# Kernel optimization log

Measured on AMD Instinct MI355X. Metric: run time of the kernel, lower is better.

Reference implementation:

```python
import jax, jax.numpy as jnp
import numpy as np

NEG = -9.0e9  # the -9000000000.0 sentinel used by the torch code


def _masked_bidir_scores(first, second, fmask, smask):
    """Vectorized form of the BxB python double loop in score_grounding.
    first: (B,N,D), second: (B,L,D), fmask: (B,N), smask: (B,L).
    Returns sent_scores (B,B) and mention_scores (B,N,L) (= diagonal att)."""
    mask = fmask[:, None, :, None] * smask[None, :, None, :]          # (B,B,N,L)
    avg = jnp.where(mask != 0, mask, NEG)
    am_first = jax.nn.softmax(avg, axis=2)                            # softmax over N (dim=0 per pair)
    am_second = jax.nn.softmax(avg, axis=3)                           # softmax over L (dim=1 per pair)
    dot = jnp.einsum('ind,jld->ijnl', first, second)                  # (B,B,N,L)
    attm = dot * mask
    att = jnp.where(attm * mask != 0, attm, NEG)
    aw_first = jax.nn.softmax(att, axis=3) * mask                     # softmax(att, dim=-1)*mask
    aw_second = jnp.transpose(
        jax.nn.softmax(jnp.swapaxes(att, 2, 3), axis=3) * jnp.swapaxes(mask, 2, 3), (0, 1, 3, 2)
    )                                                                 # softmax(att.T,-1)*mask.T, transposed back
    sent = (jnp.sum(aw_first * att * am_first, axis=(2, 3))
            + jnp.sum(aw_second * att * am_second, axis=(2, 3)))      # (B,B)
    B = first.shape[0]
    mention = att[jnp.arange(B), jnp.arange(B)]                       # diagonal pairs (B,N,L)
    return sent, mention


def _pairwise_mlp(first, second, W1, b1, W2, b2, W3, b3):
    # SimplePairWiseClassifier: MLP over cat(first, second, first*second); dropout=0 (eval-deterministic)
    x = jnp.concatenate([first, second, first * second], axis=-1)     # (..., 3D)
    h = jax.nn.relu(x @ W1 + b1)
    h = jax.nn.relu(h @ W2 + b2)
    return (h @ W3 + b3)[..., 0]


def setup_inputs() -> dict:
    key = jax.random.key(0)
    ks = jax.random.split(key, 12)
    B, Nt, Ns, L, D, H = 32, 64, 48, 36, 1024, 1024

    def mask(k, n):
        m = (jax.random.uniform(k, (B, n)) < 0.85).astype(jnp.float32)
        return m.at[:, :2].set(1.0)  # guarantee no all-zero rows

    return {
        'text_embeddings': jax.random.normal(ks[0], (B, Nt, D), jnp.float32),
        'span_embeddings': jax.random.normal(ks[1], (B, Ns, D), jnp.float32),
        'image_embeddings': jax.random.normal(ks[2], (B, L, D), jnp.float32),
        'text_mask': mask(ks[3], Nt),
        'span_mask': mask(ks[4], Ns),
        'image_mask': mask(ks[5], L),
        'W1': jax.random.normal(ks[6], (3 * D, H), jnp.float32) * 0.02,
        'b1': jnp.zeros((H,), jnp.float32),
        'W2': jax.random.normal(ks[7], (H, H), jnp.float32) * 0.02,
        'b2': jnp.zeros((H,), jnp.float32),
        'W3': jax.random.normal(ks[8], (H, 1), jnp.float32) * 0.02,
        'b3': jnp.zeros((1,), jnp.float32),
    }


def reference(text_embeddings, span_embeddings, image_embeddings,
              text_mask, span_mask, image_mask, W1, b1, W2, b2, W3, b3):
    B, Ns, D = span_embeddings.shape
    # calculate_loss
    S, _ = _masked_bidir_scores(text_embeddings, image_embeddings, text_mask, image_mask)
    # span_emb.view(B, N, -1, D).mean(dim=2) is identity for (B,Ns,D)
    _, grounding_scores = _masked_bidir_scores(span_embeddings, image_embeddings, span_mask, image_mask)
    # score_text over all span pairs (itertools.combinations order == triu_indices k=1)
    fi, si = np.triu_indices(Ns, k=1)
    text_scores = _pairwise_mlp(span_embeddings[:, fi], span_embeddings[:, si],
                                W1, b1, W2, b2, W3, b3)               # (B, Ns*(Ns-1)/2)
    # contrastive retrieval loss over the BxB sentence-image score matrix
    loss = -(jnp.trace(jax.nn.log_softmax(S, axis=1))
             + jnp.trace(jax.nn.log_softmax(S.T, axis=1))) / B
    return loss, grounding_scores, text_scores
```

## Files before the change

### kernel.cpp

```cpp
#include <hip/hip_runtime.h>
#include <math.h>
#include <stdint.h>

#define B_    32
#define NT    64
#define NS    48
#define LI    36
#define D_    1024
#define H_    1024
#define NPAIR 1128
#define ROWS  (B_*NPAIR)
#define NEGV  -9.0e9f
#define NROWT 282
#define CPX   36

typedef _Float16 half8 __attribute__((ext_vector_type(8)));
typedef float floatx4 __attribute__((ext_vector_type(4)));
typedef __attribute__((address_space(3))) uint32_t lds_u32;
typedef __attribute__((address_space(1))) const uint32_t glb_u32;

#define GLOAD16(src, dst) __builtin_amdgcn_global_load_lds((glb_u32*)(src), (lds_u32*)(dst), 16, 0, 0)

template<int EPI, int REMAP>
__global__ __launch_bounds__(256) void mfma_gemm(
    const _Float16* __restrict__ A, const _Float16* __restrict__ Bt,
    float* __restrict__ Cf, float* __restrict__ scores,
    const float* __restrict__ bias, const float* __restrict__ W3,
    int N, int K) {
  __shared__ __align__(16) _Float16 sA[8192];
  __shared__ __align__(16) _Float16 sB[8192];
  __shared__ float sRed[128][2];
  int rowT, colT;
  if (REMAP) {
    int bid = blockIdx.x;
    int x = bid & 7, ord = bid >> 3;
    rowT = x * CPX + (ord >> 3);
    colT = ord & 7;
    if (rowT >= NROWT) return;
  } else {
    rowT = blockIdx.y; colT = blockIdx.x;
  }
  const int rowBase = rowT * 128, colBase = colT * 128;
  const int tid = threadIdx.x;
  const int lane = tid & 63;
  const int wave = tid >> 6;
  const int wr = wave >> 1, wc = wave & 1;
  const int l15 = lane & 15, l16 = lane >> 4;

  const int sRow = tid >> 2;
  const int sCol = (tid & 3) << 3;
  const _Float16* gA = A + (size_t)(rowBase + sRow) * K + sCol;
  const _Float16* gB = Bt + (size_t)(colBase + sRow) * K + sCol;
  _Float16* lA = sA + tid * 8;
  _Float16* lB = sB + tid * 8;

  floatx4 acc[4][4] = {};
  for (int k0 = 0; k0 < K; k0 += 64) {
    GLOAD16(gA + k0,              lA);
    GLOAD16(gA + 64 * K + k0,     lA + 2048);
    GLOAD16(gA + k0 + 32,         lA + 4096);
    GLOAD16(gA + 64 * K + k0 + 32,lA + 6144);
    GLOAD16(gB + k0,              lB);
    GLOAD16(gB + 64 * K + k0,     lB + 2048);
    GLOAD16(gB + k0 + 32,         lB + 4096);
    GLOAD16(gB + 64 * K + k0 + 32,lB + 6144);
    __syncthreads();
#pragma unroll
    for (int h = 0; h < 2; ++h) {
      const int hb = h * 4096;
      half8 aF[4], bF[4];
#pragma unroll
      for (int i = 0; i < 4; ++i)
        aF[i] = *(const half8*)&sA[hb + (wr * 64 + i * 16 + l15) * 32 + l16 * 8];
#pragma unroll
      for (int j = 0; j < 4; ++j)
        bF[j] = *(const half8*)&sB[hb + (wc * 64 + j * 16 + l15) * 32 + l16 * 8];
#pragma unroll
      for (int i = 0; i < 4; ++i)
#pragma unroll
        for (int j = 0; j < 4; ++j)
          acc[i][j] = __builtin_amdgcn_mfma_f32_16x16x32_f16(aF[i], bF[j], acc[i][j], 0, 0, 0);
    }
    __syncthreads();
  }

  if (EPI == 0) {
#pragma unroll
    for (int i = 0; i < 4; ++i)
#pragma unroll
      for (int q = 0; q < 4; ++q) {
        int r = rowBase + wr * 64 + i * 16 + l16 * 4 + q;
#pragma unroll
        for (int j = 0; j < 4; ++j) {
          int c = colBase + wc * 64 + j * 16 + l15;
          Cf[(size_t)r * N + c] = acc[i][j][q];
        }
      }
  } else {
    float bv[4], wv[4];
#pragma unroll
    for (int j = 0; j < 4; ++j) {
      int c = colBase + wc * 64 + j * 16 + l15;
      bv[j] = bias[c];
      wv[j] = W3[c];
    }
#pragma unroll
    for (int i = 0; i < 4; ++i)
#pragma unroll
      for (int q = 0; q < 4; ++q) {
        float s = 0.f;
#pragma unroll
        for (int j = 0; j < 4; ++j) s += fmaxf(acc[i][j][q] + bv[j], 0.f) * wv[j];
        s += __shfl_xor(s, 1); s += __shfl_xor(s, 2);
        s += __shfl_xor(s, 4); s += __shfl_xor(s, 8);
        if (l15 == 0) sRed[wr * 64 + i * 16 + l16 * 4 + q][wc] = s;
      }
    __syncthreads();
    if (tid < 128)
      atomicAdd(&scores[rowBase + tid], sRed[tid][0] + sRed[tid][1]);
  }
}

__global__ __launch_bounds__(256) void gemm1_fused(
    const _Float16* __restrict__ spanH, const _Float16* __restrict__ W1cT,
    const float* __restrict__ AB1, const float* __restrict__ b1,
    _Float16* __restrict__ h1out,
    const int* __restrict__ idxF, const int* __restrict__ idxS) {
  __shared__ __align__(16) _Float16 sA[8192];
  __shared__ __align__(16) _Float16 sB[8192];
  __shared__ int sIF[128], sIS[128];
  int bid = blockIdx.x;
  int x = bid & 7, ord = bid >> 3;
  int rowT = x * CPX + (ord >> 3);
  int colT = ord & 7;
  if (rowT >= NROWT) return;
  const int rowBase = rowT * 128, colBase = colT * 128;
  const int tid = threadIdx.x;
  const int lane = tid & 63;
  const int wave = tid >> 6;
  const int wr = wave >> 1, wc = wave & 1;
  const int l15 = lane & 15, l16 = lane >> 4;

  if (tid < 128) {
    int rg = rowBase + tid;
    sIF[tid] = idxF[rg];
    sIS[tid] = idxS[rg];
  }
  __syncthreads();

  const int sRow = tid >> 2;
  const int sCol = (tid & 3) << 3;
  const _Float16* gB = W1cT + (size_t)(colBase + sRow) * D_ + sCol;
  _Float16* lB = sB + tid * 8;
  const _Float16* pf0 = spanH + (size_t)sIF[sRow] * D_ + sCol;
  const _Float16* ps0 = spanH + (size_t)sIS[sRow] * D_ + sCol;
  const _Float16* pf1 = spanH + (size_t)sIF[sRow + 64] * D_ + sCol;
  const _Float16* ps1 = spanH + (size_t)sIS[sRow + 64] * D_ + sCol;

  floatx4 acc[4][4] = {};
  for (int k0 = 0; k0 < D_; k0 += 64) {
    GLOAD16(gB + k0,               lB);
    GLOAD16(gB + 64 * D_ + k0,     lB + 2048);
    GLOAD16(gB + k0 + 32,          lB + 4096);
    GLOAD16(gB + 64 * D_ + k0 + 32,lB + 6144);
    half8 f00 = *(const half8*)(pf0 + k0);
    half8 s00 = *(const half8*)(ps0 + k0);
    half8 f10 = *(const half8*)(pf1 + k0);
    half8 s10 = *(const half8*)(ps1 + k0);
    half8 f01 = *(const half8*)(pf0 + k0 + 32);
    half8 s01 = *(const half8*)(ps0 + k0 + 32);
    half8 f11 = *(const half8*)(pf1 + k0 + 32);
    half8 s11 = *(const half8*)(ps1 + k0 + 32);
    *(half8*)(sA + tid * 8)        = f00 * s00;
    *(half8*)(sA + 2048 + tid * 8) = f10 * s10;
    *(half8*)(sA + 4096 + tid * 8) = f01 * s01;
    *(half8*)(sA + 6144 + tid * 8) = f11 * s11;
    __syncthreads();
#pragma unroll
    for (int h = 0; h < 2; ++h) {
      const int hb = h * 4096;
      half8 aF[4], bF[4];
#pragma unroll
      for (int i = 0; i < 4; ++i)
        aF[i] = *(const half8*)&sA[hb + (wr * 64 + i * 16 + l15) * 32 + l16 * 8];
#pragma unroll
      for (int j = 0; j < 4; ++j)
        bF[j] = *(const half8*)&sB[hb + (wc * 64 + j * 16 + l15) * 32 + l16 * 8];
#pragma unroll
      for (int i = 0; i < 4; ++i)
#pragma unroll
        for (int j = 0; j < 4; ++j)
          acc[i][j] = __builtin_amdgcn_mfma_f32_16x16x32_f16(aF[i], bF[j], acc[i][j], 0, 0, 0);
    }
    __syncthreads();
  }

  int cols[4]; float bv[4];
#pragma unroll
  for (int j = 0; j < 4; ++j) {
    cols[j] = colBase + wc * 64 + j * 16 + l15;
    bv[j] = b1[cols[j]];
  }
#pragma unroll
  for (int i = 0; i < 4; ++i)
#pragma unroll
    for (int q = 0; q < 4; ++q) {
      int rL = wr * 64 + i * 16 + l16 * 4 + q;
      int rG = rowBase + rL;
      const float* ap = AB1 + (size_t)sIF[rL] * 2048;
      const float* bp = AB1 + (size_t)sIS[rL] * 2048 + 1024;
#pragma unroll
      for (int j = 0; j < 4; ++j) {
        int c = cols[j];
        float v = acc[i][j][q] + ap[c] + bp[c] + bv[j];
        h1out[(size_t)rG * 1024 + c] = (_Float16)fmaxf(v, 0.f);
      }
    }
}

__global__ __launch_bounds__(256) void cvt_f16(
    const float* __restrict__ in, _Float16* __restrict__ out, long long n8) {
  long long i = (long long)blockIdx.x * 256 + threadIdx.x;
  if (i >= n8) return;
  const float4* p = (const float4*)in + i * 2;
  float4 a = p[0], b = p[1];
  half8 h;
  h[0] = (_Float16)a.x; h[1] = (_Float16)a.y; h[2] = (_Float16)a.z; h[3] = (_Float16)a.w;
  h[4] = (_Float16)b.x; h[5] = (_Float16)b.y; h[6] = (_Float16)b.z; h[7] = (_Float16)b.w;
  *(half8*)(out + i * 8) = h;
}

__global__ __launch_bounds__(256) void transpose_cvt(
    const float* __restrict__ in, _Float16* __restrict__ out) {
  __shared__ float t[32][33];
  const int tx = threadIdx.x & 31, ty = threadIdx.x >> 5;
  const int k0 = blockIdx.y * 32, n0 = blockIdx.x * 32;
#pragma unroll
  for (int q = 0; q < 4; ++q)
    t[ty + q * 8][tx] = in[(size_t)(k0 + ty + q * 8) * 1024 + n0 + tx];
  __syncthreads();
#pragma unroll
  for (int q = 0; q < 4; ++q)
    out[(size_t)(n0 + ty + q * 8) * 1024 + k0 + tx] = (_Float16)t[tx][ty + q * 8];
}

__global__ __launch_bounds__(256) void idx_init(int* __restrict__ idxF, int* __restrict__ idxS) {
  int r = blockIdx.x * 256 + threadIdx.x;
  if (r >= ROWS) return;
  int bb = r / NPAIR, p = r - bb * NPAIR;
  int cum = 0, f = 0;
  while (true) { int cnt = NS - 1 - f; if (p < cum + cnt) break; cum += cnt; ++f; }
  idxF[r] = bb * NS + f;
  idxS[r] = bb * NS + f + 1 + (p - cum);
}

__global__ void init_scores(float* __restrict__ scores, const float* __restrict__ b3) {
  int idx = blockIdx.x * 256 + threadIdx.x;
  if (idx < ROWS) scores[idx] = b3[0];
}

__global__ __launch_bounds__(256) void extract_grounding(
    const float* __restrict__ dotSI, const float* __restrict__ smask,
    const float* __restrict__ imask, float* __restrict__ outg) {
  int idx = blockIdx.x * 256 + threadIdx.x;
  if (idx >= B_ * NS * LI) return;
  int b = idx / (NS * LI);
  int rem = idx - b * (NS * LI);
  int n = rem / LI, l = rem - n * LI;
  float v = dotSI[(size_t)(b * NS + n) * (B_ * LI) + b * LI + l];
  outg[idx] = (smask[b * NS + n] * imask[b * LI + l] != 0.f) ? v : NEGV;
}

__global__ __launch_bounds__(64) void sent_kernel(
    const float* __restrict__ dotTI, const float* __restrict__ tmask,
    const float* __restrict__ imask, float* __restrict__ S) {
  const int i = blockIdx.y, j = blockIdx.x, t = threadIdx.x;
  __shared__ float red1[64], red2[64];
  const int stride = B_ * LI;
  float e1 = 0.f;
  {
    float tm = tmask[i * NT + t];
    if (tm != 0.f) {
      const float* row = dotTI + (size_t)(i * NT + t) * stride + j * LI;
      float m = -INFINITY;
      for (int l = 0; l < LI; ++l) if (imask[j * LI + l] != 0.f) m = fmaxf(m, row[l]);
      float z = 0.f, w = 0.f;
      for (int l = 0; l < LI; ++l) if (imask[j * LI + l] != 0.f) {
        float d = row[l], p = expf(d - m);
        z += p; w += p * d;
      }
      e1 = w / z;
    }
  }
  red1[t] = e1;
  float e2 = 0.f;
  if (t < LI) {
    float im = imask[j * LI + t];
    if (im != 0.f) {
      const float* col = dotTI + (size_t)(i * NT) * stride + j * LI + t;
      float m = -INFINITY;
      for (int n = 0; n < NT; ++n) if (tmask[i * NT + n] != 0.f) m = fmaxf(m, col[(size_t)n * stride]);
      float z = 0.f, w = 0.f;
      for (int n = 0; n < NT; ++n) if (tmask[i * NT + n] != 0.f) {
        float d = col[(size_t)n * stride], p = expf(d - m);
        z += p; w += p * d;
      }
      e2 = w / z;
    }
  }
  red2[t] = e2;
  __syncthreads();
  if (t == 0) {
    float s1 = 0.f, s2 = 0.f, cn = 0.f, cl = 0.f;
    for (int n = 0; n < NT; ++n) { s1 += red1[n]; cn += tmask[i * NT + n]; }
    for (int l = 0; l < LI; ++l) { s2 += red2[l]; cl += imask[j * LI + l]; }
    S[i * B_ + j] = s1 / cn + s2 / cl;
  }
}

__global__ __launch_bounds__(64) void loss_kernel(
    const float* __restrict__ S, float* __restrict__ out) {
  __shared__ float sS[B_][B_ + 1];
  __shared__ float acc[B_];
  const int t = threadIdx.x;
  for (int e = t; e < B_ * B_; e += 64) sS[e / B_][e % B_] = S[e];
  __syncthreads();
  if (t < B_) {
    float m = -INFINITY;
    for (int j = 0; j < B_; ++j) m = fmaxf(m, sS[t][j]);
    float z = 0.f;
    for (int j = 0; j < B_; ++j) z += expf(sS[t][j] - m);
    float lr = m + logf(z);
    float m2 = -INFINITY;
    for (int i = 0; i < B_; ++i) m2 = fmaxf(m2, sS[i][t]);
    float z2 = 0.f;
    for (int i = 0; i < B_; ++i) z2 += expf(sS[i][t] - m2);
    float lc = m2 + logf(z2);
    acc[t] = 2.f * sS[t][t] - lr - lc;
  }
  __syncthreads();
  if (t == 0) {
    float s = 0.f;
    for (int i = 0; i < B_; ++i) s += acc[i];
    out[0] = -s / (float)B_;
  }
}

extern "C" void kernel_launch(void* const* d_in, const int* in_sizes, int n_in,
                              void* d_out, int out_size, void* d_ws, size_t ws_size,
                              hipStream_t stream) {
  const float* text  = (const float*)d_in[0];
  const float* span  = (const float*)d_in[1];
  const float* img   = (const float*)d_in[2];
  const float* tmask = (const float*)d_in[3];
  const float* smask = (const float*)d_in[4];
  const float* imask = (const float*)d_in[5];
  const float* W1    = (const float*)d_in[6];
  const float* b1    = (const float*)d_in[7];
  const float* W2    = (const float*)d_in[8];
  const float* b2    = (const float*)d_in[9];
  const float* W3    = (const float*)d_in[10];
  const float* b3    = (const float*)d_in[11];

  float* out     = (float*)d_out;
  float* outLoss = out;
  float* outG    = out + 1;
  float* outT    = out + 1 + (size_t)B_ * NS * LI;

  char* w = (char*)d_ws;
  float*    dotTI = (float*)w;            w += (size_t)(B_*NT) * (B_*LI) * 4;
  float*    dotSI = (float*)w;            w += (size_t)(B_*NS) * (B_*LI) * 4;
  float*    S     = (float*)w;            w += 1024 * 4;
  float*    AB1   = (float*)w;            w += (size_t)1536 * 2048 * 4;
  _Float16* h1    = (_Float16*)w;         w += (size_t)ROWS * 1024 * 2;
  _Float16* textH = (_Float16*)w;         w += (size_t)2048 * 1024 * 2;
  _Float16* spanH = (_Float16*)w;         w += (size_t)1536 * 1024 * 2;
  _Float16* imgH  = (_Float16*)w;         w += (size_t)1152 * 1024 * 2;
  _Float16* W1abT = (_Float16*)w;         w += (size_t)2048 * 1024 * 2;
  _Float16* W1cT  = (_Float16*)w;         w += (size_t)1024 * 1024 * 2;
  _Float16* W2T   = (_Float16*)w;         w += (size_t)1024 * 1024 * 2;
  int*      idxF  = (int*)w;              w += ROWS * 4;
  int*      idxS  = (int*)w;              w += ROWS * 4;
  (void)ws_size; (void)in_sizes; (void)n_in; (void)out_size;

  cvt_f16<<<(2048 * 128 + 255) / 256, 256, 0, stream>>>(text, textH, 2048LL * 128);
  cvt_f16<<<(1536 * 128 + 255) / 256, 256, 0, stream>>>(span, spanH, 1536LL * 128);
  cvt_f16<<<(1152 * 128 + 255) / 256, 256, 0, stream>>>(img, imgH, 1152LL * 128);
  transpose_cvt<<<dim3(32, 32), 256, 0, stream>>>(W1, W1abT);
  transpose_cvt<<<dim3(32, 32), 256, 0, stream>>>(W1 + 1024 * 1024, W1abT + 1024 * 1024);
  transpose_cvt<<<dim3(32, 32), 256, 0, stream>>>(W1 + 2048 * 1024, W1cT);
  transpose_cvt<<<dim3(32, 32), 256, 0, stream>>>(W2, W2T);
  idx_init<<<(ROWS + 255) / 256, 256, 0, stream>>>(idxF, idxS);

  mfma_gemm<0, 0><<<dim3((B_*LI) / 128, (B_*NT) / 128), 256, 0, stream>>>(
      textH, imgH, dotTI, nullptr, nullptr, nullptr, B_ * LI, D_);
  sent_kernel<<<dim3(B_, B_), 64, 0, stream>>>(dotTI, tmask, imask, S);
  loss_kernel<<<1, 64, 0, stream>>>(S, outLoss);

  mfma_gemm<0, 0><<<dim3((B_*LI) / 128, (B_*NS) / 128), 256, 0, stream>>>(
      spanH, imgH, dotSI, nullptr, nullptr, nullptr, B_ * LI, D_);
  extract_grounding<<<(B_*NS*LI + 255) / 256, 256, 0, stream>>>(dotSI, smask, imask, outG);

  mfma_gemm<0, 0><<<dim3(2048 / 128, 1536 / 128), 256, 0, stream>>>(
      spanH, W1abT, AB1, nullptr, nullptr, nullptr, 2048, D_);

  gemm1_fused<<<8 * CPX * 8, 256, 0, stream>>>(
      spanH, W1cT, AB1, b1, h1, idxF, idxS);

  init_scores<<<(ROWS + 255) / 256, 256, 0, stream>>>(outT, b3);
  mfma_gemm<2, 1><<<8 * CPX * 8, 256, 0, stream>>>(
      h1, W2T, nullptr, outT, b2, W3, 1024, H_);
}
```

Before: 362.8 us.

## XOR-swizzle LDS tiles and stream gathered span rows via direct global-to-LDS loads

```diff
diff --git a/kernel.cpp b/kernel.cpp
--- a/kernel.cpp
+++ b/kernel.cpp
@@ -20,6 +20,7 @@
 typedef __attribute__((address_space(1))) const uint32_t glb_u32;
 
 #define GLOAD16(src, dst) __builtin_amdgcn_global_load_lds((glb_u32*)(src), (lds_u32*)(dst), 16, 0, 0)
+
 
 template<int EPI, int REMAP>
 __global__ __launch_bounds__(256) void mfma_gemm(
@@ -46,24 +47,25 @@
   const int wave = tid >> 6;
   const int wr = wave >> 1, wc = wave & 1;
   const int l15 = lane & 15, l16 = lane >> 4;
+  const int rsw = (l15 >> 1) & 3;
 
   const int sRow = tid >> 2;
-  const int sCol = (tid & 3) << 3;
-  const _Float16* gA = A + (size_t)(rowBase + sRow) * K + sCol;
-  const _Float16* gB = Bt + (size_t)(colBase + sRow) * K + sCol;
+  const int swz8 = (((tid & 3) ^ ((tid >> 3) & 3)) << 3);
+  const _Float16* gA = A + (size_t)(rowBase + sRow) * K + swz8;
+  const _Float16* gB = Bt + (size_t)(colBase + sRow) * K + swz8;
   _Float16* lA = sA + tid * 8;
   _Float16* lB = sB + tid * 8;
 
   floatx4 acc[4][4] = {};
   for (int k0 = 0; k0 < K; k0 += 64) {
-    GLOAD16(gA + k0,              lA);
-    GLOAD16(gA + 64 * K + k0,     lA + 2048);
-    GLOAD16(gA + k0 + 32,         lA + 4096);
-    GLOAD16(gA + 64 * K + k0 + 32,lA + 6144);
-    GLOAD16(gB + k0,              lB);
-    GLOAD16(gB + 64 * K + k0,     lB + 2048);
-    GLOAD16(gB + k0 + 32,         lB + 4096);
-    GLOAD16(gB + 64 * K + k0 + 32,lB + 6144);
+    GLOAD16(gA + k0,               lA);
+    GLOAD16(gA + 64 * K + k0,      lA + 2048);
+    GLOAD16(gA + k0 + 32,          lA + 4096);
+    GLOAD16(gA + 64 * K + k0 + 32, lA + 6144);
+    GLOAD16(gB + k0,               lB);
+    GLOAD16(gB + 64 * K + k0,      lB + 2048);
+    GLOAD16(gB + k0 + 32,          lB + 4096);
+    GLOAD16(gB + 64 * K + k0 + 32, lB + 6144);
     __syncthreads();
 #pragma unroll
     for (int h = 0; h < 2; ++h) {
@@ -71,10 +73,10 @@
       half8 aF[4], bF[4];
 #pragma unroll
       for (int i = 0; i < 4; ++i)
-        aF[i] = *(const half8*)&sA[hb + (wr * 64 + i * 16 + l15) * 32 + l16 * 8];
+        aF[i] = *(const half8*)&sA[hb + (wr * 64 + i * 16 + l15) * 32 + ((l16 ^ rsw) << 3)];
 #pragma unroll
       for (int j = 0; j < 4; ++j)
-        bF[j] = *(const half8*)&sB[hb + (wc * 64 + j * 16 + l15) * 32 + l16 * 8];
+        bF[j] = *(const half8*)&sB[hb + (wc * 64 + j * 16 + l15) * 32 + ((l16 ^ rsw) << 3)];
 #pragma unroll
       for (int i = 0; i < 4; ++i)
 #pragma unroll
@@ -126,7 +128,8 @@
     const float* __restrict__ AB1, const float* __restrict__ b1,
     _Float16* __restrict__ h1out,
     const int* __restrict__ idxF, const int* __restrict__ idxS) {
-  __shared__ __align__(16) _Float16 sA[8192];
+  __shared__ __align__(16) _Float16 sF[8192];
+  __shared__ __align__(16) _Float16 sS[8192];
   __shared__ __align__(16) _Float16 sB[8192];
   __shared__ int sIF[128], sIS[128];
   int bid = blockIdx.x;
@@ -140,6 +143,7 @@
   const int wave = tid >> 6;
   const int wr = wave >> 1, wc = wave & 1;
   const int l15 = lane & 15, l16 = lane >> 4;
+  const int rsw = (l15 >> 1) & 3;
 
   if (tid < 128) {
     int rg = rowBase + tid;
@@ -149,43 +153,45 @@
   __syncthreads();
 
   const int sRow = tid >> 2;
-  const int sCol = (tid & 3) << 3;
-  const _Float16* gB = W1cT + (size_t)(colBase + sRow) * D_ + sCol;
+  const int swz8 = (((tid & 3) ^ ((tid >> 3) & 3)) << 3);
+  const _Float16* gF0 = spanH + (size_t)sIF[sRow] * D_ + swz8;
+  const _Float16* gF1 = spanH + (size_t)sIF[sRow + 64] * D_ + swz8;
+  const _Float16* gS0 = spanH + (size_t)sIS[sRow] * D_ + swz8;
+  const _Float16* gS1 = spanH + (size_t)sIS[sRow + 64] * D_ + swz8;
+  const _Float16* gB  = W1cT + (size_t)(colBase + sRow) * D_ + swz8;
+  _Float16* lF = sF + tid * 8;
+  _Float16* lS = sS + tid * 8;
   _Float16* lB = sB + tid * 8;
-  const _Float16* pf0 = spanH + (size_t)sIF[sRow] * D_ + sCol;
-  const _Float16* ps0 = spanH + (size_t)sIS[sRow] * D_ + sCol;
-  const _Float16* pf1 = spanH + (size_t)sIF[sRow + 64] * D_ + sCol;
-  const _Float16* ps1 = spanH + (size_t)sIS[sRow + 64] * D_ + sCol;
 
   floatx4 acc[4][4] = {};
   for (int k0 = 0; k0 < D_; k0 += 64) {
+    GLOAD16(gF0 + k0,      lF);
+    GLOAD16(gF1 + k0,      lF + 2048);
+    GLOAD16(gF0 + k0 + 32, lF + 4096);
+    GLOAD16(gF1 + k0 + 32, lF + 6144);
+    GLOAD16(gS0 + k0,      lS);
+    GLOAD16(gS1 + k0,      lS + 2048);
+    GLOAD16(gS0 + k0 + 32, lS + 4096);
+    GLOAD16(gS1 + k0 + 32, lS + 6144);
     GLOAD16(gB + k0,               lB);
     GLOAD16(gB + 64 * D_ + k0,     lB + 2048);
     GLOAD16(gB + k0 + 32,          lB + 4096);
     GLOAD16(gB + 64 * D_ + k0 + 32,lB + 6144);
-    half8 f00 = *(const half8*)(pf0 + k0);
-    half8 s00 = *(const half8*)(ps0 + k0);
-    half8 f10 = *(const half8*)(pf1 + k0);
-    half8 s10 = *(const half8*)(ps1 + k0);
-    half8 f01 = *(const half8*)(pf0 + k0 + 32);
-    half8 s01 = *(const half8*)(ps0 + k0 + 32);
-    half8 f11 = *(const half8*)(pf1 + k0 + 32);
-    half8 s11 = *(const half8*)(ps1 + k0 + 32);
-    *(half8*)(sA + tid * 8)        = f00 * s00;
-    *(half8*)(sA + 2048 + tid * 8) = f10 * s10;
-    *(half8*)(sA + 4096 + tid * 8) = f01 * s01;
-    *(half8*)(sA + 6144 + tid * 8) = f11 * s11;
     __syncthreads();
 #pragma unroll
     for (int h = 0; h < 2; ++h) {
       const int hb = h * 4096;
       half8 aF[4], bF[4];
 #pragma unroll
-      for (int i = 0; i < 4; ++i)
-        aF[i] = *(const half8*)&sA[hb + (wr * 64 + i * 16 + l15) * 32 + l16 * 8];
+      for (int i = 0; i < 4; ++i) {
+        int off = hb + (wr * 64 + i * 16 + l15) * 32 + ((l16 ^ rsw) << 3);
+        half8 f = *(const half8*)&sF[off];
+        half8 s = *(const half8*)&sS[off];
+        aF[i] = f * s;
+      }
 #pragma unroll
       for (int j = 0; j < 4; ++j)
-        bF[j] = *(const half8*)&sB[hb + (wc * 64 + j * 16 + l15) * 32 + l16 * 8];
+        bF[j] = *(const half8*)&sB[hb + (wc * 64 + j * 16 + l15) * 32 + ((l16 ^ rsw) << 3)];
 #pragma unroll
       for (int i = 0; i < 4; ++i)
 #pragma unroll
```

Result: faster. 354.1 us (-2.4%).
